# Optimization experiments

Measured on AMD Instinct MI355X. Metric: run time of the kernel, lower is better.

The kernel has to match this reference:

```python
import jax, jax.numpy as jnp
import numpy as np

N, E, D_IN, D_OUT = 50000, 800000, 128, 128


def setup_inputs() -> dict:
    key = jax.random.key(0)
    ks = jax.random.split(key, 4)
    x = jax.random.normal(ks[0], (N, D_IN), jnp.float32)
    edge_index = jax.random.randint(ks[1], (2, E), 0, N)
    # GCNConv.lin weight (no bias in lin; bias added after aggregation)
    W = jax.random.normal(ks[2], (D_IN, D_OUT), jnp.float32) / np.sqrt(D_IN)
    b = jnp.zeros((D_OUT,), jnp.float32)
    # edge_weight_predictor: Linear(2*dim_in, 1)
    w_pred = jax.random.normal(ks[3], (2 * D_IN, 1), jnp.float32) / np.sqrt(2 * D_IN)
    b_pred = jnp.zeros((1,), jnp.float32)
    return {"x": x, "edge_index": edge_index, "W": W, "b": b,
            "w_pred": w_pred, "b_pred": b_pred}


def reference(x, edge_index, W, b, w_pred, b_pred):
    n = x.shape[0]
    src, tgt = edge_index[0], edge_index[1]

    # --- learned edge weights: gather, concat, linear, sigmoid ---
    eemb = jnp.concatenate([x[src], x[tgt]], axis=1)          # [E, 2D]
    ew = jax.nn.sigmoid(eemb @ w_pred + b_pred)[:, 0]         # [E]

    # --- GCNConv with edge_weight (PyG gcn_norm: add self-loops w=1) ---
    loop = jnp.arange(n)
    row = jnp.concatenate([src, loop])                        # message sources
    col = jnp.concatenate([tgt, loop])                        # aggregation targets
    w_full = jnp.concatenate([ew, jnp.ones((n,), ew.dtype)])

    deg = jax.ops.segment_sum(w_full, col, num_segments=n)    # weighted in-degree
    dis = jnp.where(deg > 0, jax.lax.rsqrt(deg), 0.0)         # deg^{-1/2}, inf->0
    norm = dis[row] * w_full * dis[col]                       # [E+N]

    xw = x @ W                                                # [N, D_OUT]
    msg = norm[:, None] * xw[row]                             # [E+N, D_OUT]
    out = jax.ops.segment_sum(msg, col, num_segments=n) + b   # [N, D_OUT]
    return out
```

## Files before the change

kernel.cpp:

```cpp
#include <hip/hip_runtime.h>
#include <math.h>

#define D 128
#define GR 32
#define NC 16

__device__ __forceinline__ unsigned int bf16_round(float f) {
  unsigned int u = __float_as_uint(f);
  return (u + 0x7fffu + ((u >> 16) & 1u)) >> 16;
}
__device__ __forceinline__ float bf_lo(unsigned int u) { return __uint_as_float(u << 16); }
__device__ __forceinline__ float bf_hi(unsigned int u) { return __uint_as_float(u & 0xffff0000u); }

__global__ __launch_bounds__(256) void k_pq(const float* __restrict__ x,
                                            const float* __restrict__ w_pred,
                                            float* __restrict__ p, float* __restrict__ q,
                                            int n) {
  int wid = (blockIdx.x * blockDim.x + threadIdx.x) >> 6;
  int lane = threadIdx.x & 63;
  if (wid >= n) return;
  float2 xv = ((const float2*)(x + (size_t)wid * D))[lane];
  float2 wp = ((const float2*)w_pred)[lane];
  float2 wq = ((const float2*)w_pred)[64 + lane];
  float pp = xv.x * wp.x + xv.y * wp.y;
  float qq = xv.x * wq.x + xv.y * wq.y;
#pragma unroll
  for (int off = 32; off > 0; off >>= 1) {
    pp += __shfl_down(pp, off);
    qq += __shfl_down(qq, off);
  }
  if (lane == 0) { p[wid] = pp; q[wid] = qq; }
}

__global__ __launch_bounds__(256) void k_ew_hist(const int* __restrict__ src,
                                                 const int* __restrict__ tgt,
                                                 const float* __restrict__ p,
                                                 const float* __restrict__ q,
                                                 const float* __restrict__ b_pred,
                                                 float* __restrict__ ew,
                                                 int* __restrict__ rank,
                                                 int* __restrict__ partial,
                                                 int E, int n) {
  int e = blockIdx.x * blockDim.x + threadIdx.x;
  if (e >= E) return;
  int s = src[e], t = tgt[e];
  float z = p[s] + q[t] + b_pred[0];
  ew[e] = 1.0f / (1.0f + expf(-z));
  int c = (e >> 8) & (NC - 1);
  rank[e] = atomicAdd(&partial[c * n + t], 1);
}

__global__ __launch_bounds__(256) void k_scan1(const int* __restrict__ partial,
                                               int* __restrict__ rowptr,
                                               int* __restrict__ bsum, int n) {
  __shared__ int wsum[4];
  int base = blockIdx.x * 1024 + threadIdx.x * 4;
  int4 v = make_int4(0, 0, 0, 0);
  if (base + 3 < n) {
#pragma unroll
    for (int c = 0; c < NC; ++c) {
      int4 t = *(const int4*)(partial + (size_t)c * n + base);
      v.x += t.x; v.y += t.y; v.z += t.z; v.w += t.w;
    }
  } else {
#pragma unroll
    for (int c = 0; c < NC; ++c) {
      const int* pc = partial + (size_t)c * n;
      if (base + 0 < n) v.x += pc[base + 0];
      if (base + 1 < n) v.y += pc[base + 1];
      if (base + 2 < n) v.z += pc[base + 2];
      if (base + 3 < n) v.w += pc[base + 3];
    }
  }
  int s = v.x + v.y + v.z + v.w;
  int lane = threadIdx.x & 63;
  int wave = threadIdx.x >> 6;
  int incl = s;
#pragma unroll
  for (int off = 1; off < 64; off <<= 1) {
    int t = __shfl_up(incl, off);
    if (lane >= off) incl += t;
  }
  if (lane == 63) wsum[wave] = incl;
  __syncthreads();
  int woff = 0;
#pragma unroll
  for (int w = 0; w < 4; ++w) if (w < wave) woff += wsum[w];
  int excl = woff + incl - s;
  if (base + 0 < n) rowptr[base + 0] = excl;
  if (base + 1 < n) rowptr[base + 1] = excl + v.x;
  if (base + 2 < n) rowptr[base + 2] = excl + v.x + v.y;
  if (base + 3 < n) rowptr[base + 3] = excl + v.x + v.y + v.z;
  if (threadIdx.x == 255) bsum[blockIdx.x] = woff + incl;
}

__global__ __launch_bounds__(64) void k_scan2(const int* __restrict__ bsum,
                                              int* __restrict__ bpre, int nb) {
  int lane = threadIdx.x;
  int v = (lane < nb) ? bsum[lane] : 0;
  int incl = v;
#pragma unroll
  for (int off = 1; off < 64; off <<= 1) {
    int t = __shfl_up(incl, off);
    if (lane >= off) incl += t;
  }
  if (lane < nb) bpre[lane] = incl - v;
}

__global__ __launch_bounds__(256) void k_cursors(int* __restrict__ rowptr,
                                                 const int* __restrict__ bpre,
                                                 const int* __restrict__ partial,
                                                 int* __restrict__ cursor,
                                                 int n, int E) {
  int t = blockIdx.x * blockDim.x + threadIdx.x;
  if (t < n) {
    int r = rowptr[t] + bpre[t >> 10];
    rowptr[t] = r;
#pragma unroll
    for (int c = 0; c < NC; ++c) {
      cursor[c * n + t] = r;
      r += partial[c * n + t];
    }
  }
  if (t == 0) rowptr[n] = E;
}

__global__ __launch_bounds__(256) void k_fill(const int* __restrict__ src,
                                              const int* __restrict__ tgt,
                                              const float* __restrict__ ew,
                                              const int* __restrict__ rank,
                                              const int* __restrict__ cursor,
                                              int2* __restrict__ epair, int E, int n) {
  int e = blockIdx.x * blockDim.x + threadIdx.x;
  if (e >= E) return;
  int s = src[e], t = tgt[e];
  int c = (e >> 8) & (NC - 1);
  int pos = cursor[c * n + t] + rank[e];
  epair[pos] = make_int2(s, __float_as_int(ew[e]));
}

__global__ __launch_bounds__(256) void k_deg(const int* __restrict__ rowptr,
                                             const int2* __restrict__ epair,
                                             float* __restrict__ dis, int n) {
  int t = blockIdx.x * blockDim.x + threadIdx.x;
  if (t >= n) return;
  int beg = rowptr[t], end = rowptr[t + 1];
  float s = 1.0f;
  for (int j = beg; j < end; ++j) s += __int_as_float(epair[j].y);
  dis[t] = (s > 0.0f) ? rsqrtf(s) : 0.0f;
}

__global__ __launch_bounds__(256) void k_gemm(const float* __restrict__ x,
                                              const float* __restrict__ W,
                                              const float* __restrict__ dis,
                                              unsigned int* __restrict__ xwh, int n) {
  __shared__ float Ws[64 * D];
  __shared__ float xs[GR * D];

  int row0 = blockIdx.x * GR;
  float4* xs4 = (float4*)xs;
  const float4* x4 = (const float4*)x;
  for (int i = threadIdx.x; i < GR * D / 4; i += 256) {
    int r = i >> 5;
    int gr = row0 + r;
    xs4[i] = (gr < n) ? x4[(size_t)gr * 32 + (i & 31)] : make_float4(0.f, 0.f, 0.f, 0.f);
  }

  int colg = threadIdx.x & 31;
  int rowg = threadIdx.x >> 5;
  float4 acc[4];
#pragma unroll
  for (int r = 0; r < 4; ++r) acc[r] = make_float4(0.f, 0.f, 0.f, 0.f);

  const float4* W4 = (const float4*)W;
  float4* Ws4 = (float4*)Ws;

  for (int half = 0; half < 2; ++half) {
    __syncthreads();
    for (int i = threadIdx.x; i < 64 * D / 4; i += 256)
      Ws4[i] = W4[half * (64 * D / 4) + i];
    __syncthreads();
#pragma unroll
    for (int k4 = 0; k4 < 16; ++k4) {
      float4 xv[4];
#pragma unroll
      for (int r = 0; r < 4; ++r)
        xv[r] = xs4[(rowg * 4 + r) * 32 + half * 16 + k4];
#pragma unroll
      for (int kk = 0; kk < 4; ++kk) {
        float4 w = Ws4[(k4 * 4 + kk) * 32 + colg];
#pragma unroll
        for (int r = 0; r < 4; ++r) {
          float xk = (&xv[r].x)[kk];
          acc[r].x = fmaf(xk, w.x, acc[r].x);
          acc[r].y = fmaf(xk, w.y, acc[r].y);
          acc[r].z = fmaf(xk, w.z, acc[r].z);
          acc[r].w = fmaf(xk, w.w, acc[r].w);
        }
      }
    }
  }

#pragma unroll
  for (int r = 0; r < 4; ++r) {
    int gr = row0 + rowg * 4 + r;
    if (gr < n) {
      float dv = dis[gr];
      uint2 pk;
      pk.x = bf16_round(acc[r].x * dv) | (bf16_round(acc[r].y * dv) << 16);
      pk.y = bf16_round(acc[r].z * dv) | (bf16_round(acc[r].w * dv) << 16);
      *(uint2*)(xwh + (size_t)gr * 64 + colg * 2) = pk;
    }
  }
}

__global__ __launch_bounds__(256) void k_gather(const int* __restrict__ rowptr,
                                                const int2* __restrict__ epair,
                                                const uint4* __restrict__ xwh4,
                                                const float* __restrict__ dis,
                                                const float* __restrict__ b,
                                                float* __restrict__ out, int n) {
  int wid = (blockIdx.x * blockDim.x + threadIdx.x) >> 6;
  int lane = threadIdx.x & 63;
  if (wid >= n) return;
  int cj = lane & 15;
  int rg = lane >> 4;
  int beg = rowptr[wid], end = rowptr[wid + 1];

  float acc[8];
  if (rg == 0) {
    uint4 v = xwh4[(size_t)wid * 16 + cj];
    acc[0] = bf_lo(v.x); acc[1] = bf_hi(v.x);
    acc[2] = bf_lo(v.y); acc[3] = bf_hi(v.y);
    acc[4] = bf_lo(v.z); acc[5] = bf_hi(v.z);
    acc[6] = bf_lo(v.w); acc[7] = bf_hi(v.w);
  } else {
#pragma unroll
    for (int i = 0; i < 8; ++i) acc[i] = 0.0f;
  }

  for (int j0 = beg; j0 < end; j0 += 64) {
    int m = end - j0; if (m > 64) m = 64;
    int2 pr = make_int2(0, 0);
    if (lane < m) pr = epair[j0 + lane];
    for (int k = 0; k < m; k += 4) {
      int idx = k + rg;
      int s = __shfl(pr.x, idx);
      float c = __int_as_float(__shfl(pr.y, idx));
      if (idx >= m) { s = 0; c = 0.0f; }
      uint4 v = xwh4[(size_t)s * 16 + cj];
      acc[0] = fmaf(c, bf_lo(v.x), acc[0]);
      acc[1] = fmaf(c, bf_hi(v.x), acc[1]);
      acc[2] = fmaf(c, bf_lo(v.y), acc[2]);
      acc[3] = fmaf(c, bf_hi(v.y), acc[3]);
      acc[4] = fmaf(c, bf_lo(v.z), acc[4]);
      acc[5] = fmaf(c, bf_hi(v.z), acc[5]);
      acc[6] = fmaf(c, bf_lo(v.w), acc[6]);
      acc[7] = fmaf(c, bf_hi(v.w), acc[7]);
    }
  }

#pragma unroll
  for (int i = 0; i < 8; ++i) {
    acc[i] += __shfl_xor(acc[i], 16);
    acc[i] += __shfl_xor(acc[i], 32);
  }

  if (rg == 0) {
    float dt = dis[wid];
    float4 b0 = ((const float4*)b)[cj * 2];
    float4 b1 = ((const float4*)b)[cj * 2 + 1];
    float4 o0, o1;
    o0.x = fmaf(dt, acc[0], b0.x); o0.y = fmaf(dt, acc[1], b0.y);
    o0.z = fmaf(dt, acc[2], b0.z); o0.w = fmaf(dt, acc[3], b0.w);
    o1.x = fmaf(dt, acc[4], b1.x); o1.y = fmaf(dt, acc[5], b1.y);
    o1.z = fmaf(dt, acc[6], b1.z); o1.w = fmaf(dt, acc[7], b1.w);
    ((float4*)out)[(size_t)wid * 32 + cj * 2] = o0;
    ((float4*)out)[(size_t)wid * 32 + cj * 2 + 1] = o1;
  }
}

extern "C" void kernel_launch(void* const* d_in, const int* in_sizes, int n_in,
                              void* d_out, int out_size, void* d_ws, size_t ws_size,
                              hipStream_t stream) {
  const float* x      = (const float*)d_in[0];
  const int*   ei     = (const int*)d_in[1];
  const float* W      = (const float*)d_in[2];
  const float* b      = (const float*)d_in[3];
  const float* w_pred = (const float*)d_in[4];
  const float* b_pred = (const float*)d_in[5];

  int n = in_sizes[0] / D;
  int E = in_sizes[1] / 2;
  const int* src = ei;
  const int* tgt = ei + E;

  float* out = (float*)d_out;
  float* ws  = (float*)d_ws;
  unsigned int* xwh = (unsigned int*)ws;
  float* p       = ws + (size_t)n * 64;
  float* q       = p + n;
  float* dis     = q + n;
  float* ew      = dis + n;
  int*   rank    = (int*)(ew + E);
  int2*  epair   = (int2*)(rank + E);
  int*   partial = (int*)(epair + E);
  int*   cursor  = partial + (size_t)NC * n;
  int*   rowptr  = cursor + (size_t)NC * n;
  int*   bsum    = rowptr + n + 1;
  int*   bpre    = bsum + 64;

  int nb = (n + 1023) / 1024;

  (void)hipMemsetAsync(partial, 0, (size_t)NC * n * sizeof(int), stream);
  k_pq<<<(n + 3) / 4, 256, 0, stream>>>(x, w_pred, p, q, n);
  k_ew_hist<<<(E + 255) / 256, 256, 0, stream>>>(src, tgt, p, q, b_pred, ew, rank, partial, E, n);
  k_scan1<<<nb, 256, 0, stream>>>(partial, rowptr, bsum, n);
  k_scan2<<<1, 64, 0, stream>>>(bsum, bpre, nb);
  k_cursors<<<(n + 255) / 256, 256, 0, stream>>>(rowptr, bpre, partial, cursor, n, E);
  k_fill<<<(E + 255) / 256, 256, 0, stream>>>(src, tgt, ew, rank, cursor, epair, E, n);
  k_deg<<<(n + 255) / 256, 256, 0, stream>>>(rowptr, epair, dis, n);
  k_gemm<<<(n + GR - 1) / GR, 256, 0, stream>>>(x, W, dis, xwh, n);
  k_gather<<<(n + 3) / 4, 256, 0, stream>>>(rowptr, epair, (const uint4*)xwh, dis, b, out, n);
}
```

Measured before the change: 220.2 us.

## Compute edge weights per target node after CSR fill and fold scan2 into cursors

Edge-weight sigmoid computation moves out of the histogram pass into a new per-node wave kernel that runs after the CSR fill. It writes weights in CSR order and computes the degree and its inverse square root with a wave reduction, replacing the serial per-thread degree loop. The fill kernel now scatters only source indices, into a separate array from the weights. The single-wave block-prefix scan is merged into the cursor kernel, so each block redoes it in shared memory and one launch is dropped. The intent is to cut launch count, random scatter width and the serial degree loop, at the cost of an extra gather of p[src] in CSR order.

```diff
diff --git a/kernel.cpp b/kernel.cpp
--- a/kernel.cpp
+++ b/kernel.cpp
@@ -32,20 +32,13 @@
   if (lane == 0) { p[wid] = pp; q[wid] = qq; }
 }
 
-__global__ __launch_bounds__(256) void k_ew_hist(const int* __restrict__ src,
-                                                 const int* __restrict__ tgt,
-                                                 const float* __restrict__ p,
-                                                 const float* __restrict__ q,
-                                                 const float* __restrict__ b_pred,
-                                                 float* __restrict__ ew,
-                                                 int* __restrict__ rank,
-                                                 int* __restrict__ partial,
-                                                 int E, int n) {
+__global__ __launch_bounds__(256) void k_hist(const int* __restrict__ tgt,
+                                              int* __restrict__ rank,
+                                              int* __restrict__ partial,
+                                              int E, int n) {
   int e = blockIdx.x * blockDim.x + threadIdx.x;
   if (e >= E) return;
-  int s = src[e], t = tgt[e];
-  float z = p[s] + q[t] + b_pred[0];
-  ew[e] = 1.0f / (1.0f + expf(-z));
+  int t = tgt[e];
   int c = (e >> 8) & (NC - 1);
   rank[e] = atomicAdd(&partial[c * n + t], 1);
 }
@@ -94,27 +87,27 @@
   if (threadIdx.x == 255) bsum[blockIdx.x] = woff + incl;
 }
 
-__global__ __launch_bounds__(64) void k_scan2(const int* __restrict__ bsum,
-                                              int* __restrict__ bpre, int nb) {
-  int lane = threadIdx.x;
-  int v = (lane < nb) ? bsum[lane] : 0;
-  int incl = v;
-#pragma unroll
-  for (int off = 1; off < 64; off <<= 1) {
-    int t = __shfl_up(incl, off);
-    if (lane >= off) incl += t;
-  }
-  if (lane < nb) bpre[lane] = incl - v;
-}
-
 __global__ __launch_bounds__(256) void k_cursors(int* __restrict__ rowptr,
-                                                 const int* __restrict__ bpre,
+                                                 const int* __restrict__ bsum,
                                                  const int* __restrict__ partial,
                                                  int* __restrict__ cursor,
-                                                 int n, int E) {
+                                                 int n, int E, int nb) {
+  __shared__ int bpre_s[64];
+  if (threadIdx.x < 64) {
+    int lane = threadIdx.x;
+    int v = (lane < nb) ? bsum[lane] : 0;
+    int incl = v;
+#pragma unroll
+    for (int off = 1; off < 64; off <<= 1) {
+      int t = __shfl_up(incl, off);
+      if (lane >= off) incl += t;
+    }
+    bpre_s[lane] = incl - v;
+  }
+  __syncthreads();
   int t = blockIdx.x * blockDim.x + threadIdx.x;
   if (t < n) {
-    int r = rowptr[t] + bpre[t >> 10];
+    int r = rowptr[t] + bpre_s[t >> 10];
     rowptr[t] = r;
 #pragma unroll
     for (int c = 0; c < NC; ++c) {
@@ -127,27 +120,47 @@
 
 __global__ __launch_bounds__(256) void k_fill(const int* __restrict__ src,
                                               const int* __restrict__ tgt,
-                                              const float* __restrict__ ew,
                                               const int* __restrict__ rank,
                                               const int* __restrict__ cursor,
-                                              int2* __restrict__ epair, int E, int n) {
+                                              int* __restrict__ ecol, int E, int n) {
   int e = blockIdx.x * blockDim.x + threadIdx.x;
   if (e >= E) return;
-  int s = src[e], t = tgt[e];
+  int t = tgt[e];
   int c = (e >> 8) & (NC - 1);
   int pos = cursor[c * n + t] + rank[e];
-  epair[pos] = make_int2(s, __float_as_int(ew[e]));
-}
-
-__global__ __launch_bounds__(256) void k_deg(const int* __restrict__ rowptr,
-                                             const int2* __restrict__ epair,
-                                             float* __restrict__ dis, int n) {
-  int t = blockIdx.x * blockDim.x + threadIdx.x;
-  if (t >= n) return;
-  int beg = rowptr[t], end = rowptr[t + 1];
-  float s = 1.0f;
-  for (int j = beg; j < end; ++j) s += __int_as_float(epair[j].y);
-  dis[t] = (s > 0.0f) ? rsqrtf(s) : 0.0f;
+  ecol[pos] = src[e];
+}
+
+__global__ __launch_bounds__(256) void k_node(const int* __restrict__ rowptr,
+                                              const int* __restrict__ ecol,
+                                              const float* __restrict__ p,
+                                              const float* __restrict__ q,
+                                              const float* __restrict__ b_pred,
+                                              float* __restrict__ ewt,
+                                              float* __restrict__ dis, int n) {
+  int wid = (blockIdx.x * blockDim.x + threadIdx.x) >> 6;
+  int lane = threadIdx.x & 63;
+  if (wid >= n) return;
+  int beg = rowptr[wid], end = rowptr[wid + 1];
+  float qt = q[wid] + b_pred[0];
+  float sum = 0.0f;
+  for (int j0 = beg; j0 < end; j0 += 64) {
+    int j = j0 + lane;
+    float w = 0.0f;
+    if (j < end) {
+      int s = ecol[j];
+      float z = p[s] + qt;
+      w = 1.0f / (1.0f + expf(-z));
+      ewt[j] = w;
+    }
+    sum += w;
+  }
+#pragma unroll
+  for (int off = 32; off > 0; off >>= 1) sum += __shfl_down(sum, off);
+  if (lane == 0) {
+    float d = 1.0f + sum;
+    dis[wid] = (d > 0.0f) ? rsqrtf(d) : 0.0f;
+  }
 }
 
 __global__ __launch_bounds__(256) void k_gemm(const float* __restrict__ x,
@@ -215,7 +228,8 @@
 }
 
 __global__ __launch_bounds__(256) void k_gather(const int* __restrict__ rowptr,
-                                                const int2* __restrict__ epair,
+                                                const int* __restrict__ ecol,
+                                                const float* __restrict__ ewt,
                                                 const uint4* __restrict__ xwh4,
                                                 const float* __restrict__ dis,
                                                 const float* __restrict__ b,
@@ -241,12 +255,12 @@
 
   for (int j0 = beg; j0 < end; j0 += 64) {
     int m = end - j0; if (m > 64) m = 64;
-    int2 pr = make_int2(0, 0);
-    if (lane < m) pr = epair[j0 + lane];
+    int sl = 0; float cl = 0.0f;
+    if (lane < m) { sl = ecol[j0 + lane]; cl = ewt[j0 + lane]; }
     for (int k = 0; k < m; k += 4) {
       int idx = k + rg;
-      int s = __shfl(pr.x, idx);
-      float c = __int_as_float(__shfl(pr.y, idx));
+      int s = __shfl(sl, idx);
+      float c = __shfl(cl, idx);
       if (idx >= m) { s = 0; c = 0.0f; }
       uint4 v = xwh4[(size_t)s * 16 + cj];
       acc[0] = fmaf(c, bf_lo(v.x), acc[0]);
@@ -301,25 +315,23 @@
   float* p       = ws + (size_t)n * 64;
   float* q       = p + n;
   float* dis     = q + n;
-  float* ew      = dis + n;
-  int*   rank    = (int*)(ew + E);
-  int2*  epair   = (int2*)(rank + E);
-  int*   partial = (int*)(epair + E);
+  float* ewt     = dis + n;
+  int*   ecol    = (int*)(ewt + E);
+  int*   rank    = ecol + E;
+  int*   partial = rank + E;
   int*   cursor  = partial + (size_t)NC * n;
   int*   rowptr  = cursor + (size_t)NC * n;
   int*   bsum    = rowptr + n + 1;
-  int*   bpre    = bsum + 64;
 
   int nb = (n + 1023) / 1024;
 
   (void)hipMemsetAsync(partial, 0, (size_t)NC * n * sizeof(int), stream);
   k_pq<<<(n + 3) / 4, 256, 0, stream>>>(x, w_pred, p, q, n);
-  k_ew_hist<<<(E + 255) / 256, 256, 0, stream>>>(src, tgt, p, q, b_pred, ew, rank, partial, E, n);
+  k_hist<<<(E + 255) / 256, 256, 0, stream>>>(tgt, rank, partial, E, n);
   k_scan1<<<nb, 256, 0, stream>>>(partial, rowptr, bsum, n);
-  k_scan2<<<1, 64, 0, stream>>>(bsum, bpre, nb);
-  k_cursors<<<(n + 255) / 256, 256, 0, stream>>>(rowptr, bpre, partial, cursor, n, E);
-  k_fill<<<(E + 255) / 256, 256, 0, stream>>>(src, tgt, ew, rank, cursor, epair, E, n);
-  k_deg<<<(n + 255) / 256, 256, 0, stream>>>(rowptr, epair, dis, n);
+  k_cursors<<<(n + 255) / 256, 256, 0, stream>>>(rowptr, bsum, partial, cursor, n, E, nb);
+  k_fill<<<(E + 255) / 256, 256, 0, stream>>>(src, tgt, rank, cursor, ecol, E, n);
+  k_node<<<(n + 3) / 4, 256, 0, stream>>>(rowptr, ecol, p, q, b_pred, ewt, dis, n);
   k_gemm<<<(n + GR - 1) / GR, 256, 0, stream>>>(x, W, dis, xwh, n);
-  k_gather<<<(n + 3) / 4, 256, 0, stream>>>(rowptr, epair, (const uint4*)xwh, dis, b, out, n);
-}
+  k_gather<<<(n + 3) / 4, 256, 0, stream>>>(rowptr, ecol, ewt, (const uint4*)xwh, dis, b, out, n);
+}
```

After: 224.3 us. About the same (+1.9%).
